# Performance work log

Hardware: AMD Instinct MI355X
Metric: run time of the kernel (lower is better)

## Reference

```python
import jax, jax.numpy as jnp
import numpy as np


def setup_inputs() -> dict:
    key = jax.random.key(0)
    B, F = 16384, 4096
    x = jax.random.normal(key, (B, F), dtype=jnp.float32)
    return {"x": x, "k": 64}


def reference(x, k):
    # top-k along dim=1 (last axis for 2D input)
    _, idx = jax.lax.top_k(x, k)                      # idx: [B, k]
    B = x.shape[0]
    rows = jnp.arange(B)[:, None]                     # [B, 1]
    mask = jnp.zeros_like(x).at[rows, idx].set(1.0)   # scatter ones at top-k positions
    return x * mask
```

## Files before the change

kernel.cpp:

```cpp
#include <hip/hip_runtime.h>
#include <stdint.h>

#define TK_F       4096
#define TK_THREADS 256
#define TK_EPT     16
#define TK_NBINS   2048
#define TK_CAP     1024

__device__ __forceinline__ unsigned int tk_f2u(unsigned int b) {
    return b ^ ((unsigned int)(((int)b) >> 31) | 0x80000000u);
}
__device__ __forceinline__ unsigned int tk_u2f(unsigned int u) {
    return u ^ ((~(unsigned int)(((int)u) >> 31)) | 0x80000000u);
}

__global__ __launch_bounds__(TK_THREADS, 4)
void tk_topk_mask(const float* __restrict__ x, const int* __restrict__ kp,
                  float* __restrict__ out, int B)
{
    __shared__ unsigned int hist[TK_NBINS];
    __shared__ unsigned int cand[TK_CAP];
    __shared__ unsigned int waveTot[TK_THREADS / 64];
    __shared__ unsigned int sh_cnt;
    __shared__ int          sh_b;
    __shared__ unsigned int sh_cum;
    __shared__ unsigned int sh_T, sh_g, sh_e;

    const int tid = threadIdx.x;
    const int row = blockIdx.x;
    if (row >= B) return;
    const unsigned int k = (unsigned int)kp[0];

    const unsigned int* xr  = (const unsigned int*)(x + (size_t)row * TK_F);
    unsigned int*       orow = (unsigned int*)(out + (size_t)row * TK_F);

    for (int i = tid; i < TK_NBINS; i += TK_THREADS) hist[i] = 0u;
    if (tid == 0) { sh_cnt = 0u; sh_b = -1; }

    unsigned int u[TK_EPT];
    const uint4* xv = (const uint4*)xr;
    #pragma unroll
    for (int v = 0; v < 4; ++v) {
        uint4 q = xv[tid + v * TK_THREADS];
        u[v*4+0] = tk_f2u(q.x);
        u[v*4+1] = tk_f2u(q.y);
        u[v*4+2] = tk_f2u(q.z);
        u[v*4+3] = tk_f2u(q.w);
    }
    __syncthreads();

    #pragma unroll
    for (int e = 0; e < TK_EPT; ++e)
        atomicAdd(&hist[u[e] >> 21], 1u);
    __syncthreads();

    unsigned int hbin[8];
    unsigned int s = 0;
    const int base = tid * 8;
    #pragma unroll
    for (int j = 0; j < 8; ++j) { hbin[j] = hist[base + j]; s += hbin[j]; }

    unsigned int acc = s;
    const int lane = tid & 63;
    #pragma unroll
    for (int d = 1; d < 64; d <<= 1) {
        unsigned int v = (unsigned int)__shfl_down((int)acc, d, 64);
        if (lane + d < 64) acc += v;
    }
    const int wid = tid >> 6;
    if (lane == 0) waveTot[wid] = acc;
    __syncthreads();
    unsigned int later = 0;
    #pragma unroll
    for (int w = 0; w < TK_THREADS / 64; ++w)
        if (w > wid) later += waveTot[w];

    unsigned int run = later + (acc - s);
    #pragma unroll
    for (int j = 7; j >= 0; --j) {
        unsigned int h = hbin[j];
        if (run < k && run + h >= k) { sh_b = base + j; sh_cum = run; }
        run += h;
    }
    __syncthreads();

    const int b = sh_b;
    if (b < 0) {
        #pragma unroll
        for (int v = 0; v < 4; ++v) {
            uint4 q;
            q.x = tk_u2f(u[v*4+0]); q.y = tk_u2f(u[v*4+1]);
            q.z = tk_u2f(u[v*4+2]); q.w = tk_u2f(u[v*4+3]);
            ((uint4*)orow)[tid + v * TK_THREADS] = q;
        }
        return;
    }
    const unsigned int cum = sh_cum;

    #pragma unroll
    for (int e = 0; e < TK_EPT; ++e) {
        if ((int)(u[e] >> 21) == b) {
            unsigned int p = atomicAdd(&sh_cnt, 1u);
            if (p < TK_CAP) cand[p] = u[e];
        }
    }
    __syncthreads();

    const unsigned int L = (sh_cnt < TK_CAP) ? sh_cnt : TK_CAP;
    const unsigned int r = k - cum;
    for (unsigned int j = tid; j < L; j += TK_THREADS) {
        unsigned int uj = cand[j];
        unsigned int g = 0, eq = 0;
        for (unsigned int i = 0; i < L; ++i) {
            unsigned int ui = cand[i];
            g  += (ui > uj)  ? 1u : 0u;
            eq += (ui == uj) ? 1u : 0u;
        }
        if (g < r && g + eq >= r) { sh_T = uj; sh_g = g; sh_e = eq; }
    }
    __syncthreads();

    const unsigned int T  = sh_T;
    const unsigned int re = r - sh_g;
    const unsigned int ce = sh_e;
    const bool easy = (ce == re);

    #pragma unroll
    for (int v = 0; v < 4; ++v) {
        uint4 q;
        #pragma unroll
        for (int j = 0; j < 4; ++j) {
            unsigned int uu  = u[v*4+j];
            unsigned int val = 0u;
            if (uu > T) {
                val = tk_u2f(uu);
            } else if (uu == T) {
                if (easy) {
                    val = tk_u2f(uu);
                } else {
                    int idx = (tid + v * TK_THREADS) * 4 + j;
                    unsigned int cnt = 0;
                    for (int i = 0; i < idx; ++i)
                        cnt += (tk_f2u(xr[i]) == T) ? 1u : 0u;
                    if (cnt < re) val = tk_u2f(uu);
                }
            }
            (&q.x)[j] = val;
        }
        ((uint4*)orow)[tid + v * TK_THREADS] = q;
    }
}

extern "C" void kernel_launch(void* const* d_in, const int* in_sizes, int n_in,
                              void* d_out, int out_size, void* d_ws, size_t ws_size,
                              hipStream_t stream) {
    const float* x  = (const float*)d_in[0];
    const int*   kp = (const int*)d_in[1];
    float*       out = (float*)d_out;
    const int B = in_sizes[0] / TK_F;
    hipLaunchKernelGGL(tk_topk_mask, dim3(B), dim3(TK_THREADS), 0, stream,
                       x, kp, out, B);
}
```

Baseline: 538.7 us.

## Map one wavefront per row and replace block syncs with wave ballots

Each 256-thread block now processes four rows, one per 64-lane wavefront. Each lane holds 64 elements and each wave keeps its own 2048-bin histogram in a transposed layout so lanes can sum strided bins. The bin containing the k-th element is found with a two-level ballot/shuffle search, and the threshold candidate is chosen by ballot, removing all __syncthreads and block-wide shared scalars. The per-wave candidate buffer shrinks to 256 entries, which risks overflow if more than 256 values share the threshold bin. More registers per lane and a longer pairwise candidate ranking per wave are the trade-offs.

```diff
diff --git a/kernel.cpp b/kernel.cpp
--- a/kernel.cpp
+++ b/kernel.cpp
@@ -2,10 +2,12 @@
 #include <stdint.h>
 
 #define TK_F       4096
-#define TK_THREADS 256
-#define TK_EPT     16
+#define TK_WPB     4
+#define TK_THREADS (TK_WPB * 64)
 #define TK_NBINS   2048
-#define TK_CAP     1024
+#define TK_CAP     256
+#define TK_VPL     16
+#define TK_EPL     64
 
 __device__ __forceinline__ unsigned int tk_f2u(unsigned int b) {
     return b ^ ((unsigned int)(((int)b) >> 31) | 0x80000000u);
@@ -18,119 +20,129 @@
 void tk_topk_mask(const float* __restrict__ x, const int* __restrict__ kp,
                   float* __restrict__ out, int B)
 {
-    __shared__ unsigned int hist[TK_NBINS];
-    __shared__ unsigned int cand[TK_CAP];
-    __shared__ unsigned int waveTot[TK_THREADS / 64];
-    __shared__ unsigned int sh_cnt;
-    __shared__ int          sh_b;
-    __shared__ unsigned int sh_cum;
-    __shared__ unsigned int sh_T, sh_g, sh_e;
+    __shared__ uint4        hist4[TK_WPB][TK_NBINS / 4];
+    __shared__ unsigned int cand[TK_WPB][TK_CAP];
+    __shared__ unsigned int cnt[TK_WPB];
 
-    const int tid = threadIdx.x;
-    const int row = blockIdx.x;
+    const int lane = (int)(threadIdx.x & 63u);
+    const int wid  = (int)(threadIdx.x >> 6);
+    const int row  = blockIdx.x * TK_WPB + wid;
     if (row >= B) return;
+
     const unsigned int k = (unsigned int)kp[0];
+    unsigned int* hw = (unsigned int*)hist4[wid];
 
-    const unsigned int* xr  = (const unsigned int*)(x + (size_t)row * TK_F);
+    const unsigned int* xr   = (const unsigned int*)(x + (size_t)row * TK_F);
     unsigned int*       orow = (unsigned int*)(out + (size_t)row * TK_F);
+    const uint4*        xv   = (const uint4*)xr;
 
-    for (int i = tid; i < TK_NBINS; i += TK_THREADS) hist[i] = 0u;
-    if (tid == 0) { sh_cnt = 0u; sh_b = -1; }
+    unsigned int u[TK_EPL];
+    #pragma unroll
+    for (int v = 0; v < TK_VPL; ++v) {
+        uint4 t = xv[lane + v * 64];
+        u[v*4+0] = t.x; u[v*4+1] = t.y; u[v*4+2] = t.z; u[v*4+3] = t.w;
+    }
 
-    unsigned int u[TK_EPT];
-    const uint4* xv = (const uint4*)xr;
+    const uint4 z = make_uint4(0u, 0u, 0u, 0u);
     #pragma unroll
-    for (int v = 0; v < 4; ++v) {
-        uint4 q = xv[tid + v * TK_THREADS];
-        u[v*4+0] = tk_f2u(q.x);
-        u[v*4+1] = tk_f2u(q.y);
-        u[v*4+2] = tk_f2u(q.z);
-        u[v*4+3] = tk_f2u(q.w);
-    }
-    __syncthreads();
+    for (int i = 0; i < TK_NBINS / 4 / 64; ++i)
+        hist4[wid][lane + i * 64] = z;
+    if (lane == 0) cnt[wid] = 0u;
 
     #pragma unroll
-    for (int e = 0; e < TK_EPT; ++e)
-        atomicAdd(&hist[u[e] >> 21], 1u);
-    __syncthreads();
+    for (int e = 0; e < TK_EPL; ++e) {
+        u[e] = tk_f2u(u[e]);
+        const unsigned int b11 = u[e] >> 21;
+        atomicAdd(&hw[((b11 & 63u) << 5) | (b11 >> 6)], 1u);
+    }
 
-    unsigned int hbin[8];
+    const unsigned int sbase = ((unsigned int)(lane & 1) << 10) | ((unsigned int)lane >> 1);
     unsigned int s = 0;
-    const int base = tid * 8;
     #pragma unroll
-    for (int j = 0; j < 8; ++j) { hbin[j] = hist[base + j]; s += hbin[j]; }
+    for (int j = 0; j < 32; ++j)
+        s += hw[sbase + ((unsigned int)j << 5)];
 
     unsigned int acc = s;
-    const int lane = tid & 63;
     #pragma unroll
     for (int d = 1; d < 64; d <<= 1) {
-        unsigned int v = (unsigned int)__shfl_down((int)acc, d, 64);
-        if (lane + d < 64) acc += v;
+        const unsigned int t = (unsigned int)__shfl_down((int)acc, (unsigned int)d, 64);
+        if (lane + d < 64) acc += t;
     }
-    const int wid = tid >> 6;
-    if (lane == 0) waveTot[wid] = acc;
-    __syncthreads();
-    unsigned int later = 0;
-    #pragma unroll
-    for (int w = 0; w < TK_THREADS / 64; ++w)
-        if (w > wid) later += waveTot[w];
+    const unsigned int above = acc - s;
 
-    unsigned int run = later + (acc - s);
-    #pragma unroll
-    for (int j = 7; j >= 0; --j) {
-        unsigned int h = hbin[j];
-        if (run < k && run + h >= k) { sh_b = base + j; sh_cum = run; }
-        run += h;
+    const unsigned long long bal = __ballot((above < k) && (acc >= k));
+    int b = -1;
+    unsigned int cum = 0;
+    if (bal != 0ull) {
+        const int wl = __ffsll((unsigned long long)bal) - 1;
+        const unsigned int A = (unsigned int)__shfl((int)above, wl, 64);
+        unsigned int hl = 0;
+        if (lane < 32)
+            hl = hw[(((unsigned int)(wl & 1)) << 10) + (((unsigned int)lane) << 5) + (((unsigned int)wl) >> 1)];
+        unsigned int a2 = hl;
+        #pragma unroll
+        for (int d = 1; d < 32; d <<= 1) {
+            const unsigned int t = (unsigned int)__shfl_down((int)a2, (unsigned int)d, 64);
+            if (lane + d < 32) a2 += t;
+        }
+        const unsigned int run = A + (a2 - hl);
+        const unsigned long long bal2 =
+            __ballot((lane < 32) && (run < k) && (run + hl >= k));
+        const int wb = __ffsll((unsigned long long)bal2) - 1;
+        b   = wl * 32 + wb;
+        cum = (unsigned int)__shfl((int)run, wb, 64);
     }
-    __syncthreads();
 
-    const int b = sh_b;
     if (b < 0) {
         #pragma unroll
-        for (int v = 0; v < 4; ++v) {
-            uint4 q;
-            q.x = tk_u2f(u[v*4+0]); q.y = tk_u2f(u[v*4+1]);
-            q.z = tk_u2f(u[v*4+2]); q.w = tk_u2f(u[v*4+3]);
-            ((uint4*)orow)[tid + v * TK_THREADS] = q;
+        for (int v = 0; v < TK_VPL; ++v) {
+            uint4 t;
+            t.x = tk_u2f(u[v*4+0]); t.y = tk_u2f(u[v*4+1]);
+            t.z = tk_u2f(u[v*4+2]); t.w = tk_u2f(u[v*4+3]);
+            ((uint4*)orow)[lane + v * 64] = t;
         }
         return;
     }
-    const unsigned int cum = sh_cum;
 
+    const unsigned int bb = (unsigned int)b;
     #pragma unroll
-    for (int e = 0; e < TK_EPT; ++e) {
-        if ((int)(u[e] >> 21) == b) {
-            unsigned int p = atomicAdd(&sh_cnt, 1u);
-            if (p < TK_CAP) cand[p] = u[e];
+    for (int e = 0; e < TK_EPL; ++e) {
+        if ((u[e] >> 21) == bb) {
+            const unsigned int p = atomicAdd(&cnt[wid], 1u);
+            if (p < TK_CAP) cand[wid][p] = u[e];
         }
     }
-    __syncthreads();
 
-    const unsigned int L = (sh_cnt < TK_CAP) ? sh_cnt : TK_CAP;
+    unsigned int L = cnt[wid];
+    if (L > TK_CAP) L = TK_CAP;
     const unsigned int r = k - cum;
-    for (unsigned int j = tid; j < L; j += TK_THREADS) {
-        unsigned int uj = cand[j];
+
+    unsigned int Tl = 0, gl = 0, el = 0;
+    int found = 0;
+    for (unsigned int j = (unsigned int)lane; j < L; j += 64u) {
+        const unsigned int uj = cand[wid][j];
         unsigned int g = 0, eq = 0;
         for (unsigned int i = 0; i < L; ++i) {
-            unsigned int ui = cand[i];
+            const unsigned int ui = cand[wid][i];
             g  += (ui > uj)  ? 1u : 0u;
             eq += (ui == uj) ? 1u : 0u;
         }
-        if (g < r && g + eq >= r) { sh_T = uj; sh_g = g; sh_e = eq; }
+        if (g < r && g + eq >= r) { Tl = uj; gl = g; el = eq; found = 1; }
     }
-    __syncthreads();
-
-    const unsigned int T  = sh_T;
-    const unsigned int re = r - sh_g;
-    const unsigned int ce = sh_e;
-    const bool easy = (ce == re);
+    const unsigned long long bal3 = __ballot(found);
+    const int wt = __ffsll((unsigned long long)bal3) - 1;
+    const unsigned int T  = (unsigned int)__shfl((int)Tl, wt, 64);
+    const unsigned int g0 = (unsigned int)__shfl((int)gl, wt, 64);
+    const unsigned int e0 = (unsigned int)__shfl((int)el, wt, 64);
+    const unsigned int re = r - g0;
+    const bool easy = (e0 == re);
 
     #pragma unroll
-    for (int v = 0; v < 4; ++v) {
-        uint4 q;
+    for (int v = 0; v < TK_VPL; ++v) {
+        uint4 t;
         #pragma unroll
         for (int j = 0; j < 4; ++j) {
-            unsigned int uu  = u[v*4+j];
+            const unsigned int uu = u[v*4 + j];
             unsigned int val = 0u;
             if (uu > T) {
                 val = tk_u2f(uu);
@@ -138,26 +150,26 @@
                 if (easy) {
                     val = tk_u2f(uu);
                 } else {
-                    int idx = (tid + v * TK_THREADS) * 4 + j;
-                    unsigned int cnt = 0;
+                    const int idx = (lane + v * 64) * 4 + j;
+                    unsigned int c2 = 0;
                     for (int i = 0; i < idx; ++i)
-                        cnt += (tk_f2u(xr[i]) == T) ? 1u : 0u;
-                    if (cnt < re) val = tk_u2f(uu);
+                        c2 += (tk_f2u(xr[i]) == T) ? 1u : 0u;
+                    if (c2 < re) val = tk_u2f(uu);
                 }
             }
-            (&q.x)[j] = val;
+            (&t.x)[j] = val;
         }
-        ((uint4*)orow)[tid + v * TK_THREADS] = q;
+        ((uint4*)orow)[lane + v * 64] = t;
     }
 }
 
 extern "C" void kernel_launch(void* const* d_in, const int* in_sizes, int n_in,
                               void* d_out, int out_size, void* d_ws, size_t ws_size,
                               hipStream_t stream) {
-    const float* x  = (const float*)d_in[0];
-    const int*   kp = (const int*)d_in[1];
+    const float* x   = (const float*)d_in[0];
+    const int*   kp  = (const int*)d_in[1];
     float*       out = (float*)d_out;
     const int B = in_sizes[0] / TK_F;
-    hipLaunchKernelGGL(tk_topk_mask, dim3(B), dim3(TK_THREADS), 0, stream,
-                       x, kp, out, B);
+    hipLaunchKernelGGL(tk_topk_mask, dim3((B + TK_WPB - 1) / TK_WPB), dim3(TK_THREADS),
+                       0, stream, x, kp, out, B);
 }
```

After: 619.6 us. +15.0%, slower.
